# Kernel tuning notes

Measured on AMD Instinct MI355X. Metric: run time of the kernel, lower is better.

Reference implementation:

```python
import jax, jax.numpy as jnp
import numpy as np

B, C, S, H, W = 1, 256, 64, 32, 128
BLOCKS, HEADS, DH = 2, 8, 32
SCALE = DH ** (-0.5)


def layer_norm(x, w, b, eps=1e-5):
    mu = jnp.mean(x, axis=-1, keepdims=True)
    var = jnp.var(x, axis=-1, keepdims=True)
    return (x - mu) * jax.lax.rsqrt(var + eps) * w + b


def generate_y_for_attn(y, u):
    # y: (B,C,H,W), u: (B,S,S) float -> (B, S^2, 2H, C)
    Bv, Cv, Hv, Wv = y.shape
    Sv = u.shape[1]
    uf = jnp.floor(u).reshape(Bv, Sv * Sv)
    u_left = jnp.clip(uf, 0, Wv - 1).astype(jnp.int32)
    u_right = jnp.clip(uf + 1, 0, Wv - 1).astype(jnp.int32)
    yf = y.reshape(Bv, Cv * Hv, Wv)

    def gather_w(idx):
        idxb = jnp.broadcast_to(idx[:, None, :], (Bv, Cv * Hv, Sv * Sv))
        return jnp.take_along_axis(yf, idxb, axis=2).reshape(Bv, Cv, Hv, Sv * Sv)

    ys = jnp.concatenate([gather_w(u_left), gather_w(u_right)], axis=2)  # (B,C,2H,S2)
    return ys.transpose(0, 3, 2, 1)  # (B, S2, 2H, C)


def cross_attention(x, y, p, i):
    # x: (B,M,C), y: (B,M,N,C)
    q = layer_norm(x, p['ln_q_w'][i], p['ln_q_b'][i]) @ p['Wq'][i]        # (B,M,HD)
    k = layer_norm(y, p['ln_k_w'][i], p['ln_k_b'][i]) @ p['Wk'][i]        # (B,M,N,HD)
    v = layer_norm(y, p['ln_v_w'][i], p['ln_v_b'][i]) @ p['Wv'][i]        # (B,M,N,HD)
    Bv, M, _ = q.shape
    N = k.shape[2]
    q = q.reshape(Bv, M, HEADS, DH)
    k = k.reshape(Bv, M, N, HEADS, DH)
    v = v.reshape(Bv, M, N, HEADS, DH)
    dot = SCALE * jnp.einsum('bmhd,bmnhd->bhmn', q, k)                    # (B,H,M,N)
    attn = jax.nn.softmax(dot, axis=-1)
    a = jnp.einsum('bhmn,bmnhd->bmhd', attn, v).reshape(Bv, M, HEADS * DH)
    z = a @ p['Wproj'][i] + p['bproj'][i]
    z = layer_norm(z, p['ln_pre_w'][i], p['ln_pre_b'][i])
    h = jax.nn.gelu(z @ p['Wm1'][i] + p['bm1'][i], approximate=False)
    z = z + (h @ p['Wm2'][i] + p['bm2'][i])
    return layer_norm(z, p['ln_post_w'][i], p['ln_post_b'][i])


def setup_inputs() -> dict:
    key = jax.random.key(0)
    ks = jax.random.split(key, 16)
    std = 0.02
    inp = {
        'grd2sat': jax.random.normal(ks[0], (B, C, S, S), jnp.float32),
        'grd_x': jax.random.normal(ks[1], (B, C, H, W), jnp.float32),
        'u': jax.random.uniform(ks[2], (B, S, S), jnp.float32) * (W - 1),
        'ln_q_w': jnp.ones((BLOCKS, C)), 'ln_q_b': jnp.zeros((BLOCKS, C)),
        'ln_k_w': jnp.ones((BLOCKS, C)), 'ln_k_b': jnp.zeros((BLOCKS, C)),
        'ln_v_w': jnp.ones((BLOCKS, C)), 'ln_v_b': jnp.zeros((BLOCKS, C)),
        'Wq': std * jax.random.normal(ks[3], (BLOCKS, C, HEADS * DH)),
        'Wk': std * jax.random.normal(ks[4], (BLOCKS, C, HEADS * DH)),
        'Wv': std * jax.random.normal(ks[5], (BLOCKS, C, HEADS * DH)),
        'Wproj': std * jax.random.normal(ks[6], (BLOCKS, HEADS * DH, C)),
        'bproj': jnp.zeros((BLOCKS, C)),
        'ln_pre_w': jnp.ones((BLOCKS, C)), 'ln_pre_b': jnp.zeros((BLOCKS, C)),
        'Wm1': std * jax.random.normal(ks[7], (BLOCKS, C, 2 * C)),
        'bm1': jnp.zeros((BLOCKS, 2 * C)),
        'Wm2': std * jax.random.normal(ks[8], (BLOCKS, 2 * C, C)),
        'bm2': jnp.zeros((BLOCKS, C)),
        'ln_post_w': jnp.ones((BLOCKS, C)), 'ln_post_b': jnp.zeros((BLOCKS, C)),
    }
    return inp


def reference(grd2sat, grd_x, u, ln_q_w, ln_q_b, ln_k_w, ln_k_b, ln_v_w, ln_v_b,
              Wq, Wk, Wv, Wproj, bproj, ln_pre_w, ln_pre_b, Wm1, bm1, Wm2, bm2,
              ln_post_w, ln_post_b):
    p = dict(ln_q_w=ln_q_w, ln_q_b=ln_q_b, ln_k_w=ln_k_w, ln_k_b=ln_k_b,
             ln_v_w=ln_v_w, ln_v_b=ln_v_b, Wq=Wq, Wk=Wk, Wv=Wv, Wproj=Wproj,
             bproj=bproj, ln_pre_w=ln_pre_w, ln_pre_b=ln_pre_b, Wm1=Wm1, bm1=bm1,
             Wm2=Wm2, bm2=bm2, ln_post_w=ln_post_w, ln_post_b=ln_post_b)
    y_attn = generate_y_for_attn(grd_x, u)               # (B, S^2, 2H, C)
    x = grd2sat.reshape(B, C, S * S).transpose(0, 2, 1)  # (B, M, C)
    for i in range(BLOCKS):
        # (Swin self-attention layer omitted; cross-attention stack only.)
        x = cross_attention(x, y_attn, p, i)
    out = x.transpose(0, 2, 1).reshape(B, C, S, S)
    # L2 normalize over channel dim
    norm = jnp.sqrt(jnp.sum(out * out, axis=1, keepdims=True))
    return out / jnp.maximum(norm, 1e-12)
```

## Files before the change

kernel.cpp:

```cpp
#include <hip/hip_runtime.h>
#include <math.h>


#define C_DIM 256
#define M_DIM 4096
#define W_DIM 128
#define H_DIM 32
#define ATT_SCALE 0.17677669529663687f

typedef __attribute__((ext_vector_type(8))) short short8;
typedef __attribute__((ext_vector_type(4))) short short4v;
typedef __attribute__((ext_vector_type(4))) float floatx4;

__device__ __forceinline__ unsigned short f2bf(float f) {
    unsigned u = __float_as_uint(f);
    unsigned r = (u + 0x7fffu + ((u >> 16) & 1u)) >> 16;
    return (unsigned short)r;
}
__device__ __forceinline__ float gelu_exact(float x) {
    return 0.5f * x * (1.0f + erff(x * 0.70710678118654752f));
}

struct PrepArgs {
    const float* grd2sat; float* xcur;
    const float* grd_x;   float* yhat;
    const float* u; int* perm; int4* chunks; int* nchunks;
    const float* win[12]; unsigned short* wout[12]; const float* wlnw[12];
    int wR[12], wC[12], wbase[13];
    const float* fW[10]; const float* flnb[10]; const float* fbase[10];
    float* fout[10];
    int fN[10], fwcol[10], focol[10];
};

__global__ __launch_bounds__(256) void prep_kernel(PrepArgs a) {
    __shared__ float smemf[9024];
    int b = blockIdx.x, t = threadIdx.x;
    if (b < 256) {
        float (*tile)[65] = (float(*)[65])smemf;
        int m0 = (b & 63) << 6, c0 = (b >> 6) << 6;
        for (int it = 0; it < 16; ++it) {
            int idx = it * 256 + t;
            int co = idx >> 6, mo = idx & 63;
            tile[co][mo] = a.grd2sat[(size_t)(c0 + co) * M_DIM + m0 + mo];
        }
        __syncthreads();
        for (int it = 0; it < 16; ++it) {
            int idx = it * 256 + t;
            int mo = idx >> 6, co = idx & 63;
            a.xcur[(size_t)(m0 + mo) * C_DIM + c0 + co] = tile[co][mo];
        }
    } else if (b < 384) {
        int idx = b - 256;
        int h = idx & 31, w0 = (idx >> 5) << 5;
        float (*tile)[33] = (float(*)[33])smemf;
        float (*ps)[32] = (float(*)[32])(smemf + 8448);
        float (*pss)[32] = (float(*)[32])(smemf + 8704);
        float* mu_s = smemf + 8960;
        float* rs_s = smemf + 8992;
        int wo = t & 31, cb = t >> 5;
        for (int it = 0; it < 32; ++it) {
            int c = it * 8 + cb;
            tile[c][wo] = a.grd_x[(size_t)c * (H_DIM * W_DIM) + h * W_DIM + w0 + wo];
        }
        __syncthreads();
        {
            int w = t & 31, part = t >> 5;
            float s = 0.f, ss = 0.f;
            for (int c = part * 32; c < part * 32 + 32; ++c) {
                float x = tile[c][w];
                s += x; ss += x * x;
            }
            ps[part][w] = s; pss[part][w] = ss;
        }
        __syncthreads();
        if (t < 32) {
            float s = 0.f, ss = 0.f;
            for (int p = 0; p < 8; ++p) { s += ps[p][t]; ss += pss[p][t]; }
            float mu = s * (1.f / 256.f);
            float var = ss * (1.f / 256.f) - mu * mu;
            mu_s[t] = mu;
            rs_s[t] = rsqrtf(var + 1e-5f);
        }
        __syncthreads();
        for (int jj = 0; jj < 32; ++jj) {
            float mu = mu_s[jj], rs = rs_s[jj];
            a.yhat[((size_t)(w0 + jj) * H_DIM + h) * C_DIM + t] =
                (tile[t][jj] - mu) * rs;
        }
    } else if (b < 1408) {
        int wI = b - 384;
        int e = 0;
        while (wI >= a.wbase[e + 1]) ++e;
        int tl = wI - a.wbase[e];
        int tilesC = a.wC[e] >> 5;
        int tr = tl / tilesC, tc = tl - tr * tilesC;
        int r0 = tr << 5, c0 = tc << 5;
        const float* in = a.win[e];
        unsigned short* out = a.wout[e];
        const float* lnw = a.wlnw[e];
        int R = a.wR[e], Cc = a.wC[e];
        float (*tile)[33] = (float(*)[33])smemf;
        int rl = t >> 3, cq = (t & 7) << 2;
        float4 v = *(const float4*)&in[(size_t)(r0 + rl) * Cc + c0 + cq];
        if (lnw) {
            float s = lnw[r0 + rl];
            v.x *= s; v.y *= s; v.z *= s; v.w *= s;
        }
        tile[rl][cq + 0] = v.x;
        tile[rl][cq + 1] = v.y;
        tile[rl][cq + 2] = v.z;
        tile[rl][cq + 3] = v.w;
        __syncthreads();
        int cl = t >> 3, rq = (t & 7) << 2;
        ushort4 o;
        o.x = f2bf(tile[rq + 0][cl]);
        o.y = f2bf(tile[rq + 1][cl]);
        o.z = f2bf(tile[rq + 2][cl]);
        o.w = f2bf(tile[rq + 3][cl]);
        *(ushort4*)&out[(size_t)(c0 + cl) * R + r0 + rq] = o;
    } else if (b < 1418) {
        int jj = b - 1408;
        int N = a.fN[jj];
        int wcol = a.fwcol[jj] + t;
        const float* W = a.fW[jj];
        const float* lb = a.flnb[jj];
        float s = a.fbase[jj] ? a.fbase[jj][wcol] : 0.f;
        for (int k = 0; k < 256; ++k) s += lb[k] * W[(size_t)k * N + wcol];
        a.fout[jj][a.focol[jj] + t] = s;
    } else {
        int* hist = (int*)smemf;
        int* cur = (int*)smemf + 128;
        unsigned short* wlb = (unsigned short*)((int*)smemf + 256);
        if (t < 128) hist[t] = 0;
        __syncthreads();
        for (int it = 0; it < 16; ++it) {
            int m = it * 256 + t;
            int wl = (int)floorf(a.u[m]);
            wl = max(0, min(wl, 126));
            wlb[m] = (unsigned short)wl;
            atomicAdd(&hist[wl], 1);
        }
        __syncthreads();
        if (t == 0) {
            int run = 0, nc = 0;
            for (int bkt = 0; bkt < 127; ++bkt) {
                int c = hist[bkt];
                cur[bkt] = run;
                int q0 = run;
                while (c > 0) {
                    int take = min(c, 32);
                    a.chunks[nc] = make_int4(bkt, q0, take, 0);
                    ++nc; q0 += take; c -= take;
                }
                run += hist[bkt];
            }
            *a.nchunks = nc;
        }
        __syncthreads();
        for (int it = 0; it < 16; ++it) {
            int m = it * 256 + t;
            int wl = wlb[m];
            int pos = atomicAdd(&cur[wl], 1);
            a.perm[pos] = m;
        }
    }
}

struct GJ {
    const void* A; const unsigned short* Bt;
    const float* bias; const float* aw; const float* ab;
    const float* rw; const float* rb; const float* res;
    float* wrz; void* out; unsigned short* out2;
    int K, N;
};

template <int LN, int EPI, int OUTM, bool WRZ, bool ABF16>
__device__ __forceinline__ void gemm_core(const GJ& j, short (*As)[264],
                                          short (*Bs)[264], int bm, int by) {
    int t = threadIdx.x;
    int bn = by << 6;
    int wv = t >> 6, lane = t & 63;
    int mt = wv & 1, nt0 = (wv >> 1) << 1;
    int quad = lane >> 4, l16 = lane & 15;
    floatx4 acc0 = {0.f, 0.f, 0.f, 0.f};
    floatx4 acc1 = {0.f, 0.f, 0.f, 0.f};
    const int K = j.K;
    for (int kc = 0; kc < K; kc += 256) {
        if (kc) __syncthreads();
        if (ABF16) {
            int ar = t >> 3, cq = (t & 7) << 5;
            const unsigned short* ap =
                (const unsigned short*)j.A + (size_t)(bm + ar) * K + kc + cq;
#pragma unroll
            for (int c = 0; c < 4; ++c)
                *(uint4*)&As[ar][cq + (c << 3)] = *(const uint4*)(ap + (c << 3));
        } else {
            int ar = t >> 3, cq = (t & 7) << 2;
            const float* ap = (const float*)j.A + (size_t)(bm + ar) * K + kc + cq;
            float4 v[8];
#pragma unroll
            for (int g = 0; g < 8; ++g) v[g] = *(const float4*)(ap + g * 32);
            if (LN >= 1) {
                float s = 0.f, ss = 0.f;
#pragma unroll
                for (int g = 0; g < 8; ++g) {
                    s += v[g].x + v[g].y + v[g].z + v[g].w;
                    ss += v[g].x * v[g].x + v[g].y * v[g].y + v[g].z * v[g].z +
                          v[g].w * v[g].w;
                }
#pragma unroll
                for (int o = 1; o < 8; o <<= 1) {
                    s += __shfl_xor(s, o, 64);
                    ss += __shfl_xor(ss, o, 64);
                }
                float mu = s * (1.f / 256.f);
                float rs = rsqrtf(ss * (1.f / 256.f) - mu * mu + 1e-5f);
#pragma unroll
                for (int g = 0; g < 8; ++g) {
                    v[g].x = (v[g].x - mu) * rs;
                    v[g].y = (v[g].y - mu) * rs;
                    v[g].z = (v[g].z - mu) * rs;
                    v[g].w = (v[g].w - mu) * rs;
                }
                if (LN == 2) {
                    float s2 = 0.f, ss2 = 0.f;
#pragma unroll
                    for (int g = 0; g < 8; ++g) {
                        float4 w4 = *(const float4*)(j.aw + cq + g * 32);
                        float4 b4 = *(const float4*)(j.ab + cq + g * 32);
                        v[g].x = v[g].x * w4.x + b4.x;
                        v[g].y = v[g].y * w4.y + b4.y;
                        v[g].z = v[g].z * w4.z + b4.z;
                        v[g].w = v[g].w * w4.w + b4.w;
                        s2 += v[g].x + v[g].y + v[g].z + v[g].w;
                        ss2 += v[g].x * v[g].x + v[g].y * v[g].y +
                               v[g].z * v[g].z + v[g].w * v[g].w;
                    }
#pragma unroll
                    for (int o = 1; o < 8; o <<= 1) {
                        s2 += __shfl_xor(s2, o, 64);
                        ss2 += __shfl_xor(ss2, o, 64);
                    }
                    float mu2 = s2 * (1.f / 256.f);
                    float rs2 = rsqrtf(ss2 * (1.f / 256.f) - mu2 * mu2 + 1e-5f);
#pragma unroll
                    for (int g = 0; g < 8; ++g) {
                        v[g].x = (v[g].x - mu2) * rs2;
                        v[g].y = (v[g].y - mu2) * rs2;
                        v[g].z = (v[g].z - mu2) * rs2;
                        v[g].w = (v[g].w - mu2) * rs2;
                    }
                }
            }
            if (WRZ) {
                if (by == 0) {
#pragma unroll
                    for (int g = 0; g < 8; ++g)
                        *(float4*)&j.wrz[(size_t)(bm + ar) * 256 + cq + g * 32] =
                            v[g];
                }
            }
#pragma unroll
            for (int g = 0; g < 8; ++g) {
                short4v o;
                o[0] = (short)f2bf(v[g].x);
                o[1] = (short)f2bf(v[g].y);
                o[2] = (short)f2bf(v[g].z);
                o[3] = (short)f2bf(v[g].w);
                *(short4v*)&As[ar][cq + g * 32] = o;
            }
        }
        {
            int br = t >> 2, cq2 = (t & 3) << 3;
            const unsigned short* bp = j.Bt + (size_t)(bn + br) * K + kc + cq2;
#pragma unroll
            for (int g = 0; g < 8; ++g)
                *(short8*)&Bs[br][cq2 + g * 32] = *(const short8*)(bp + g * 32);
        }
        __syncthreads();
#pragma unroll
        for (int k0 = 0; k0 < 8; ++k0) {
            short8 aa = *(const short8*)&As[(mt << 4) + l16][(k0 << 5) + (quad << 3)];
            short8 b0 = *(const short8*)&Bs[(nt0 << 4) + l16][(k0 << 5) + (quad << 3)];
            short8 b1 =
                *(const short8*)&Bs[((nt0 + 1) << 4) + l16][(k0 << 5) + (quad << 3)];
            acc0 = __builtin_amdgcn_mfma_f32_16x16x32_bf16(aa, b0, acc0, 0, 0, 0);
            acc1 = __builtin_amdgcn_mfma_f32_16x16x32_bf16(aa, b1, acc1, 0, 0, 0);
        }
    }
#pragma unroll
    for (int jj = 0; jj < 2; ++jj) {
        const floatx4 accv = jj ? acc1 : acc0;
        int col = bn + ((nt0 + jj) << 4) + l16;
        float bv = j.bias ? j.bias[col] : 0.f;
#pragma unroll
        for (int r = 0; r < 4; ++r) {
            int row = bm + (mt << 4) + (quad << 2) + r;
            float v = accv[r] + bv;
            if (EPI == 1) v = gelu_exact(v);
            if (EPI == 2)
                v += j.res[(size_t)row * 256 + col] * j.rw[col] + j.rb[col];
            if (OUTM == 0) {
                ((float*)j.out)[(size_t)row * j.N + col] = v;
            } else if (OUTM == 1) {
                ((unsigned short*)j.out)[(size_t)row * j.N + col] = f2bf(v);
            } else {
                if (col < 256)
                    ((unsigned short*)j.out)[(size_t)row * 256 + col] = f2bf(v);
                else
                    j.out2[(size_t)(col - 256) * M_DIM + row] = f2bf(v);
            }
        }
    }
}

template <int MODE>
__global__ __launch_bounds__(256) void gemm_mode(GJ j0, GJ j1, GJ j2) {
    __shared__ short As[32][264];
    __shared__ short Bs[64][264];
    int bm = blockIdx.x << 5;
    if (MODE == 0) {
        if ((int)blockIdx.y < 4)
            gemm_core<1, 0, 1, false, false>(j0, As, Bs, bm, blockIdx.y);
        else if ((int)blockIdx.y < 12)
            gemm_core<0, 0, 2, false, false>(j1, As, Bs, bm, blockIdx.y - 4);
        else
            gemm_core<0, 0, 2, false, false>(j2, As, Bs, bm, blockIdx.y - 12);
    } else if (MODE == 1) {
        gemm_core<2, 0, 1, false, false>(j0, As, Bs, bm, blockIdx.y);
    } else if (MODE == 2) {
        gemm_core<0, 0, 0, false, true>(j0, As, Bs, bm, blockIdx.y);
    } else if (MODE == 3) {
        gemm_core<1, 1, 1, true, false>(j0, As, Bs, bm, blockIdx.y);
    } else {
        gemm_core<0, 2, 0, false, true>(j0, As, Bs, bm, blockIdx.y);
    }
}

__global__ __launch_bounds__(256) void attn_kernel(
    const unsigned short* __restrict__ Qb, const unsigned short* __restrict__ Kt,
    const unsigned short* __restrict__ Vt, const int* __restrict__ perm,
    const int4* __restrict__ chunks, const int* __restrict__ nchunks,
    unsigned short* __restrict__ Ao) {
    __shared__ float S[32][69];
    __shared__ short Pb[32][72];
    __shared__ int gperm[32];
    if ((int)blockIdx.x >= *nchunks) return;
    int4 cd = chunks[blockIdx.x];
    int wl = cd.x, qstart = cd.y, qcnt = cd.z;
    int t = threadIdx.x;
    if (t < 32) gperm[t] = (t < qcnt) ? perm[qstart + t] : perm[qstart];
    __syncthreads();
    int wv = t >> 6, lane = t & 63, quad = lane >> 4, l16 = lane & 15;
    int mt = wv & 1, nt0 = (wv >> 1) << 1;
    int ntP = wv >> 1;
    const unsigned short* qp = Qb + (size_t)gperm[(mt << 4) + l16] * 256;
    const unsigned short* kp0 =
        Kt + ((size_t)((wl << 5) + (nt0 << 4) + l16)) * 256;
    const unsigned short* kp1 = kp0 + (16 * 256);
    int sq = t >> 3, sg = t & 7;
    int hb = (int)blockIdx.y << 2;
#pragma unroll 1
    for (int h = hb; h < hb + 4; ++h) {
        {
            short8 aa = *(const short8*)(qp + (h << 5) + (quad << 3));
            short8 b0 = *(const short8*)(kp0 + (h << 5) + (quad << 3));
            short8 b1 = *(const short8*)(kp1 + (h << 5) + (quad << 3));
            floatx4 z = {0.f, 0.f, 0.f, 0.f};
            floatx4 c0 = __builtin_amdgcn_mfma_f32_16x16x32_bf16(aa, b0, z, 0, 0, 0);
            floatx4 c1 = __builtin_amdgcn_mfma_f32_16x16x32_bf16(aa, b1, z, 0, 0, 0);
#pragma unroll
            for (int r = 0; r < 4; ++r) {
                int row = (mt << 4) + (quad << 2) + r;
                S[row][(nt0 << 4) + l16] = c0[r];
                S[row][((nt0 + 1) << 4) + l16] = c1[r];
            }
        }
        __syncthreads();
        {
            float e[8];
            float s = 0.f;
#pragma unroll
            for (int c = 0; c < 8; ++c) {
                e[c] = __expf(S[sq][(sg << 3) + c] * ATT_SCALE);
                s += e[c];
            }
            s += __shfl_xor(s, 1, 64);
            s += __shfl_xor(s, 2, 64);
            s += __shfl_xor(s, 4, 64);
            float ri = 1.f / s;
#pragma unroll
            for (int c = 0; c < 8; ++c)
                Pb[sq][(sg << 3) + c] = (short)f2bf(e[c] * ri);
        }
        __syncthreads();
        {
            const unsigned short* vp =
                Vt + ((size_t)((h << 5) + (ntP << 4) + l16)) * M_DIM + (wl << 5);
            floatx4 acc = {0.f, 0.f, 0.f, 0.f};
#pragma unroll
            for (int ks = 0; ks < 2; ++ks) {
                short8 pa =
                    *(const short8*)&Pb[(mt << 4) + l16][(ks << 5) + (quad << 3)];
                short8 vb = *(const short8*)(vp + (ks << 5) + (quad << 3));
                acc = __builtin_amdgcn_mfma_f32_16x16x32_bf16(pa, vb, acc, 0, 0, 0);
            }
#pragma unroll
            for (int r = 0; r < 4; ++r) {
                int q = (mt << 4) + (quad << 2) + r;
                if (q < qcnt)
                    Ao[(size_t)gperm[q] * 256 + (h << 5) + (ntP << 4) + l16] =
                        f2bf(acc[r]);
            }
        }
    }
}

__global__ __launch_bounds__(256) void out_kernel(const float* __restrict__ X,
                                                  const float* __restrict__ w,
                                                  const float* __restrict__ b,
                                                  float* __restrict__ out) {
    __shared__ float tile[64][65];
    int t = threadIdx.x;
    int mo = t >> 2, q = t & 3;
    int m0 = blockIdx.x << 6;
    const float* p = X + (size_t)(m0 + mo) * C_DIM + (q << 6);
    float4 v[16];
    float s = 0.f, ss = 0.f;
#pragma unroll
    for (int c = 0; c < 16; ++c) {
        v[c] = *(const float4*)(p + c * 4);
        s += v[c].x + v[c].y + v[c].z + v[c].w;
        ss += v[c].x * v[c].x + v[c].y * v[c].y + v[c].z * v[c].z + v[c].w * v[c].w;
    }
    s += __shfl_xor(s, 1, 64); s += __shfl_xor(s, 2, 64);
    ss += __shfl_xor(ss, 1, 64); ss += __shfl_xor(ss, 2, 64);
    float mu = s * (1.f / 256.f);
    float rs = rsqrtf(ss * (1.f / 256.f) - mu * mu + 1e-5f);
    float ss2 = 0.f;
#pragma unroll
    for (int c = 0; c < 16; ++c) {
        float4 w4 = *(const float4*)&w[(q << 6) + c * 4];
        float4 b4 = *(const float4*)&b[(q << 6) + c * 4];
        v[c].x = (v[c].x - mu) * rs * w4.x + b4.x;
        v[c].y = (v[c].y - mu) * rs * w4.y + b4.y;
        v[c].z = (v[c].z - mu) * rs * w4.z + b4.z;
        v[c].w = (v[c].w - mu) * rs * w4.w + b4.w;
        ss2 += v[c].x * v[c].x + v[c].y * v[c].y + v[c].z * v[c].z + v[c].w * v[c].w;
    }
    ss2 += __shfl_xor(ss2, 1, 64); ss2 += __shfl_xor(ss2, 2, 64);
    float sc = 1.f / fmaxf(sqrtf(ss2), 1e-12f);
    for (int cc = 0; cc < 4; ++cc) {
        if (q == cc) {
#pragma unroll
            for (int c = 0; c < 16; ++c) {
                tile[mo][c * 4 + 0] = v[c].x * sc;
                tile[mo][c * 4 + 1] = v[c].y * sc;
                tile[mo][c * 4 + 2] = v[c].z * sc;
                tile[mo][c * 4 + 3] = v[c].w * sc;
            }
        }
        __syncthreads();
        for (int it = 0; it < 16; ++it) {
            int idx = it * 256 + t;
            int co = idx >> 6, mr = idx & 63;
            out[(size_t)((cc << 6) + co) * M_DIM + m0 + mr] = tile[mr][co];
        }
        __syncthreads();
    }
}

extern "C" void kernel_launch(void* const* d_in, const int* in_sizes, int n_in,
                              void* d_out, int out_size, void* d_ws, size_t ws_size,
                              hipStream_t stream) {
    const float* grd2sat = (const float*)d_in[0];
    const float* grd_x   = (const float*)d_in[1];
    const float* u       = (const float*)d_in[2];
    const float* ln_q_w  = (const float*)d_in[3];
    const float* ln_q_b  = (const float*)d_in[4];
    const float* ln_k_w  = (const float*)d_in[5];
    const float* ln_k_b  = (const float*)d_in[6];
    const float* ln_v_w  = (const float*)d_in[7];
    const float* ln_v_b  = (const float*)d_in[8];
    const float* Wq      = (const float*)d_in[9];
    const float* Wk      = (const float*)d_in[10];
    const float* Wv      = (const float*)d_in[11];
    const float* Wproj   = (const float*)d_in[12];
    const float* bproj   = (const float*)d_in[13];
    const float* ln_pre_w = (const float*)d_in[14];
    const float* ln_pre_b = (const float*)d_in[15];
    const float* Wm1     = (const float*)d_in[16];
    const float* bm1     = (const float*)d_in[17];
    const float* Wm2     = (const float*)d_in[18];
    const float* bm2     = (const float*)d_in[19];
    const float* ln_post_w = (const float*)d_in[20];
    const float* ln_post_b = (const float*)d_in[21];

    float* ws   = (float*)d_ws;
    float* yhat = ws;
    float* xcur = ws + 1048576;
    float* zq   = ws + 2097152;
    float* zbuf = ws + 3145728;
    unsigned short* hbuf = (unsigned short*)(ws + 4194304);
    unsigned short* Qb   = (unsigned short*)(ws + 5242880);
    unsigned short* abuf = (unsigned short*)(ws + 5767168);
    unsigned short* Ktab0 = (unsigned short*)(ws + 6291456);
    unsigned short* Vt0   = (unsigned short*)(ws + 6815744);
    unsigned short* Ktab1 = (unsigned short*)(ws + 7340032);
    unsigned short* Vt1   = (unsigned short*)(ws + 7864320);
    unsigned short* Bt    = (unsigned short*)(ws + 8388608);
    float* biasbuf = ws + 8912896;
    int*  perm    = (int*)(ws + 8915456);
    int4* chunks  = (int4*)(ws + 8919552);
    int*  nchunks = (int*)(ws + 8921600);
    const size_t BS = 524288;
    const size_t OQ = 0, OKV = 65536, OP = 196608, OM1 = 262144, OM2 = 393216;

    dim3 b256(256);

    PrepArgs pa;
    pa.grd2sat = grd2sat; pa.xcur = xcur;
    pa.grd_x = grd_x;     pa.yhat = yhat;
    pa.u = u; pa.perm = perm; pa.chunks = chunks; pa.nchunks = nchunks;
    {
        int base = 0;
        for (int i = 0; i < 2; ++i) {
            int e = 6 * i;
            unsigned short* bt = Bt + i * BS;
            pa.win[e+0] = Wq + i * 65536;    pa.wout[e+0] = bt + OQ;
            pa.wlnw[e+0] = ln_q_w + i * 256; pa.wR[e+0] = 256; pa.wC[e+0] = 256;
            pa.win[e+1] = Wk + i * 65536;    pa.wout[e+1] = bt + OKV;
            pa.wlnw[e+1] = ln_k_w + i * 256; pa.wR[e+1] = 256; pa.wC[e+1] = 256;
            pa.win[e+2] = Wv + i * 65536;    pa.wout[e+2] = bt + OKV + 65536;
            pa.wlnw[e+2] = ln_v_w + i * 256; pa.wR[e+2] = 256; pa.wC[e+2] = 256;
            pa.win[e+3] = Wproj + i * 65536; pa.wout[e+3] = bt + OP;
            pa.wlnw[e+3] = nullptr;          pa.wR[e+3] = 256; pa.wC[e+3] = 256;
            pa.win[e+4] = Wm1 + i * 131072;  pa.wout[e+4] = bt + OM1;
            pa.wlnw[e+4] = ln_pre_w + i * 256; pa.wR[e+4] = 256; pa.wC[e+4] = 512;
            pa.win[e+5] = Wm2 + i * 131072;  pa.wout[e+5] = bt + OM2;
            pa.wlnw[e+5] = nullptr;          pa.wR[e+5] = 512; pa.wC[e+5] = 256;
        }
        for (int e = 0; e < 12; ++e) {
            pa.wbase[e] = base;
            base += (pa.wR[e] >> 5) * (pa.wC[e] >> 5);
        }
        pa.wbase[12] = base;
        for (int i = 0; i < 2; ++i) {
            int jb = 5 * i;
            float* bb = biasbuf + i * 1280;
            pa.fW[jb+0] = Wq + i * 65536; pa.flnb[jb+0] = ln_q_b + i * 256;
            pa.fbase[jb+0] = nullptr; pa.fout[jb+0] = bb;
            pa.fN[jb+0] = 256; pa.fwcol[jb+0] = 0; pa.focol[jb+0] = 0;
            pa.fW[jb+1] = Wk + i * 65536; pa.flnb[jb+1] = ln_k_b + i * 256;
            pa.fbase[jb+1] = nullptr; pa.fout[jb+1] = bb + 256;
            pa.fN[jb+1] = 256; pa.fwcol[jb+1] = 0; pa.focol[jb+1] = 0;
            pa.fW[jb+2] = Wv + i * 65536; pa.flnb[jb+2] = ln_v_b + i * 256;
            pa.fbase[jb+2] = nullptr; pa.fout[jb+2] = bb + 256;
            pa.fN[jb+2] = 256; pa.fwcol[jb+2] = 0; pa.focol[jb+2] = 256;
            pa.fW[jb+3] = Wm1 + i * 131072; pa.flnb[jb+3] = ln_pre_b + i * 256;
            pa.fbase[jb+3] = bm1 + i * 512; pa.fout[jb+3] = bb + 768;
            pa.fN[jb+3] = 512; pa.fwcol[jb+3] = 0; pa.focol[jb+3] = 0;
            pa.fW[jb+4] = Wm1 + i * 131072; pa.flnb[jb+4] = ln_pre_b + i * 256;
            pa.fbase[jb+4] = bm1 + i * 512; pa.fout[jb+4] = bb + 768;
            pa.fN[jb+4] = 512; pa.fwcol[jb+4] = 256; pa.focol[jb+4] = 256;
        }
    }
    prep_kernel<<<1419, b256, 0, stream>>>(pa);

    GJ jz = {};
    for (int i = 0; i < 2; ++i) {
        const unsigned short* bt = Bt + i * BS;
        float* bb = biasbuf + i * 1280;
        unsigned short* Kt = i ? Ktab1 : Ktab0;
        unsigned short* Vt = i ? Vt1 : Vt0;

        GJ jq = {};
        jq.A = xcur; jq.Bt = bt + OQ; jq.bias = bb;
        if (i == 1) { jq.aw = ln_post_w; jq.ab = ln_post_b; }
        jq.out = Qb; jq.K = 256; jq.N = 256;
        if (i == 0) {
            GJ jkv0 = {};
            jkv0.A = yhat; jkv0.Bt = Bt + OKV; jkv0.bias = biasbuf + 256;
            jkv0.out = Ktab0; jkv0.out2 = Vt0; jkv0.K = 256; jkv0.N = 512;
            GJ jkv1 = {};
            jkv1.A = yhat; jkv1.Bt = Bt + BS + OKV; jkv1.bias = biasbuf + 1280 + 256;
            jkv1.out = Ktab1; jkv1.out2 = Vt1; jkv1.K = 256; jkv1.N = 512;
            gemm_mode<0><<<dim3(128, 20), b256, 0, stream>>>(jq, jkv0, jkv1);
        } else {
            gemm_mode<1><<<dim3(128, 4), b256, 0, stream>>>(jq, jz, jz);
        }

        attn_kernel<<<dim3(384, 2), b256, 0, stream>>>(Qb, Kt, Vt, perm, chunks,
                                                       nchunks, abuf);

        GJ jp = {};
        jp.A = abuf; jp.Bt = bt + OP; jp.bias = bproj + i * 256;
        jp.out = zq; jp.K = 256; jp.N = 256;
        gemm_mode<2><<<dim3(128, 4), b256, 0, stream>>>(jp, jz, jz);

        GJ jm1 = {};
        jm1.A = zq; jm1.Bt = bt + OM1; jm1.bias = bb + 768;
        jm1.out = hbuf; jm1.wrz = zbuf; jm1.K = 256; jm1.N = 512;
        gemm_mode<3><<<dim3(128, 8), b256, 0, stream>>>(jm1, jz, jz);

        GJ jm2 = {};
        jm2.A = hbuf; jm2.Bt = bt + OM2; jm2.bias = bm2 + i * 256;
        jm2.res = zbuf; jm2.rw = ln_pre_w + i * 256; jm2.rb = ln_pre_b + i * 256;
        jm2.out = xcur; jm2.K = 512; jm2.N = 256;
        gemm_mode<4><<<dim3(128, 4), b256, 0, stream>>>(jm2, jz, jz);
    }
    out_kernel<<<64, b256, 0, stream>>>(xcur, ln_post_w + 256, ln_post_b + 256,
                                        (float*)d_out);
}
```

Before: 215.7 us.

## Fuse Q-proj, attention, out-proj and MLP for both blocks into one megakernel

Replaces the per-block chain of Q GEMM, attention, projection GEMM, MLP1 and MLP2 launches with a single kernel. Each workgroup owns a chunk of up to 32 query rows that share a window and keeps all intermediates in LDS across both blocks. K/V projections for both blocks are computed up front in a separate kernel. This removes many launches and the global round trips for Q, attention output, z and h. In exchange it uses about 147KB of LDS per workgroup, so occupancy is one workgroup per CU, and only 288 workgroups run, each reloading the full weight matrices.

Result: slower. 238.4 us (+10.5%).

```diff
diff --git a/kernel.cpp b/kernel.cpp
--- a/kernel.cpp
+++ b/kernel.cpp
@@ -222,43 +222,6 @@
                     v[g].z = (v[g].z - mu) * rs;
                     v[g].w = (v[g].w - mu) * rs;
                 }
-                if (LN == 2) {
-                    float s2 = 0.f, ss2 = 0.f;
-#pragma unroll
-                    for (int g = 0; g < 8; ++g) {
-                        float4 w4 = *(const float4*)(j.aw + cq + g * 32);
-                        float4 b4 = *(const float4*)(j.ab + cq + g * 32);
-                        v[g].x = v[g].x * w4.x + b4.x;
-                        v[g].y = v[g].y * w4.y + b4.y;
-                        v[g].z = v[g].z * w4.z + b4.z;
-                        v[g].w = v[g].w * w4.w + b4.w;
-                        s2 += v[g].x + v[g].y + v[g].z + v[g].w;
-                        ss2 += v[g].x * v[g].x + v[g].y * v[g].y +
-                               v[g].z * v[g].z + v[g].w * v[g].w;
-                    }
-#pragma unroll
-                    for (int o = 1; o < 8; o <<= 1) {
-                        s2 += __shfl_xor(s2, o, 64);
-                        ss2 += __shfl_xor(ss2, o, 64);
-                    }
-                    float mu2 = s2 * (1.f / 256.f);
-                    float rs2 = rsqrtf(ss2 * (1.f / 256.f) - mu2 * mu2 + 1e-5f);
-#pragma unroll
-                    for (int g = 0; g < 8; ++g) {
-                        v[g].x = (v[g].x - mu2) * rs2;
-                        v[g].y = (v[g].y - mu2) * rs2;
-                        v[g].z = (v[g].z - mu2) * rs2;
-                        v[g].w = (v[g].w - mu2) * rs2;
-                    }
-                }
-            }
-            if (WRZ) {
-                if (by == 0) {
-#pragma unroll
-                    for (int g = 0; g < 8; ++g)
-                        *(float4*)&j.wrz[(size_t)(bm + ar) * 256 + cq + g * 32] =
-                            v[g];
-                }
             }
 #pragma unroll
             for (int g = 0; g < 8; ++g) {
@@ -297,9 +260,6 @@
         for (int r = 0; r < 4; ++r) {
             int row = bm + (mt << 4) + (quad << 2) + r;
             float v = accv[r] + bv;
-            if (EPI == 1) v = gelu_exact(v);
-            if (EPI == 2)
-                v += j.res[(size_t)row * 256 + col] * j.rw[col] + j.rb[col];
             if (OUTM == 0) {
                 ((float*)j.out)[(size_t)row * j.N + col] = v;
             } else if (OUTM == 1) {
@@ -314,105 +274,368 @@
     }
 }
 
-template <int MODE>
-__global__ __launch_bounds__(256) void gemm_mode(GJ j0, GJ j1, GJ j2) {
+__global__ __launch_bounds__(256) void kv_kernel(GJ j0, GJ j1) {
     __shared__ short As[32][264];
     __shared__ short Bs[64][264];
     int bm = blockIdx.x << 5;
-    if (MODE == 0) {
-        if ((int)blockIdx.y < 4)
-            gemm_core<1, 0, 1, false, false>(j0, As, Bs, bm, blockIdx.y);
-        else if ((int)blockIdx.y < 12)
-            gemm_core<0, 0, 2, false, false>(j1, As, Bs, bm, blockIdx.y - 4);
-        else
-            gemm_core<0, 0, 2, false, false>(j2, As, Bs, bm, blockIdx.y - 12);
-    } else if (MODE == 1) {
-        gemm_core<2, 0, 1, false, false>(j0, As, Bs, bm, blockIdx.y);
-    } else if (MODE == 2) {
-        gemm_core<0, 0, 0, false, true>(j0, As, Bs, bm, blockIdx.y);
-    } else if (MODE == 3) {
-        gemm_core<1, 1, 1, true, false>(j0, As, Bs, bm, blockIdx.y);
-    } else {
-        gemm_core<0, 2, 0, false, true>(j0, As, Bs, bm, blockIdx.y);
-    }
+    if ((int)blockIdx.y < 8)
+        gemm_core<0, 0, 2, false, false>(j0, As, Bs, bm, blockIdx.y);
+    else
+        gemm_core<0, 0, 2, false, false>(j1, As, Bs, bm, blockIdx.y - 8);
 }
 
-__global__ __launch_bounds__(256) void attn_kernel(
-    const unsigned short* __restrict__ Qb, const unsigned short* __restrict__ Kt,
-    const unsigned short* __restrict__ Vt, const int* __restrict__ perm,
-    const int4* __restrict__ chunks, const int* __restrict__ nchunks,
-    unsigned short* __restrict__ Ao) {
-    __shared__ float S[32][69];
-    __shared__ short Pb[32][72];
-    __shared__ int gperm[32];
-    if ((int)blockIdx.x >= *nchunks) return;
-    int4 cd = chunks[blockIdx.x];
+struct MegaArgs {
+    const float* xcur;
+    const int* perm; const int4* chunks; const int* nchunks;
+    float* xfinal;
+    const unsigned short* Wq[2]; const unsigned short* Wp[2];
+    const unsigned short* Wm1[2]; const unsigned short* Wm2[2];
+    const unsigned short* Ktb[2]; const unsigned short* Vtb[2];
+    const float* qb[2]; const float* m1b[2];
+    const float* bpj[2]; const float* bm2v[2];
+    const float* pw[2]; const float* pb[2];
+    const float* aw; const float* ab;
+};
+
+__device__ __forceinline__ void cg_pass(const short* As, int lda,
+                                        const unsigned short* Bt, int K, int bn,
+                                        short (*Bst)[264], floatx4& acc0,
+                                        floatx4& acc1) {
+    int t = threadIdx.x;
+    int wv = t >> 6, lane = t & 63, quad = lane >> 4, l16 = lane & 15;
+    int mt = wv & 1, nt0 = (wv >> 1) << 1;
+    int br = t >> 2, cq2 = (t & 3) << 3;
+#pragma unroll 1
+    for (int kc = 0; kc < K; kc += 256) {
+        const unsigned short* bp = Bt + (size_t)(bn + br) * K + kc + cq2;
+#pragma unroll
+        for (int g = 0; g < 8; ++g)
+            *(short8*)&Bst[br][cq2 + (g << 5)] = *(const short8*)(bp + (g << 5));
+        __syncthreads();
+        const short* ap = As + (size_t)((mt << 4) + l16) * lda + kc + (quad << 3);
+#pragma unroll
+        for (int k0 = 0; k0 < 8; ++k0) {
+            short8 aa = *(const short8*)(ap + (k0 << 5));
+            short8 b0 =
+                *(const short8*)&Bst[(nt0 << 4) + l16][(k0 << 5) + (quad << 3)];
+            short8 b1 =
+                *(const short8*)&Bst[((nt0 + 1) << 4) + l16][(k0 << 5) + (quad << 3)];
+            acc0 = __builtin_amdgcn_mfma_f32_16x16x32_bf16(aa, b0, acc0, 0, 0, 0);
+            acc1 = __builtin_amdgcn_mfma_f32_16x16x32_bf16(aa, b1, acc1, 0, 0, 0);
+        }
+        __syncthreads();
+    }
+}
+
+__global__ __launch_bounds__(256) void mega_kernel(MegaArgs a) {
+    __shared__ __align__(16) char smem[150656];
+    short (*XH)[264] = (short(*)[264])(smem);
+    short (*HH)[520] = (short(*)[520])(smem);
+    short (*QR)[264] = (short(*)[264])(smem + 33280);
+    float (*Zf)[260] = (float(*)[260])(smem + 33280);
+    short (*ZH)[264] = (short(*)[264])(smem + 66560);
+    short (*AR)[264] = (short(*)[264])(smem + 83456);
+    float (*XO)[260] = (float(*)[260])(smem + 83456);
+    short (*Bst)[264] = (short(*)[264])(smem + 116736);
+    float (*SS)[69] = (float(*)[69])(smem + 116736);
+    short (*PB)[72] = (short(*)[72])(smem + 116736 + 8832);
+    int* gp = (int*)(smem + 150528);
+
+    if ((int)blockIdx.x >= *a.nchunks) return;
+    int4 cd = a.chunks[blockIdx.x];
     int wl = cd.x, qstart = cd.y, qcnt = cd.z;
     int t = threadIdx.x;
-    if (t < 32) gperm[t] = (t < qcnt) ? perm[qstart + t] : perm[qstart];
+    if (t < 32) gp[t] = (t < qcnt) ? a.perm[qstart + t] : a.perm[qstart];
     __syncthreads();
+
     int wv = t >> 6, lane = t & 63, quad = lane >> 4, l16 = lane & 15;
-    int mt = wv & 1, nt0 = (wv >> 1) << 1;
-    int ntP = wv >> 1;
-    const unsigned short* qp = Qb + (size_t)gperm[(mt << 4) + l16] * 256;
-    const unsigned short* kp0 =
-        Kt + ((size_t)((wl << 5) + (nt0 << 4) + l16)) * 256;
-    const unsigned short* kp1 = kp0 + (16 * 256);
-    int sq = t >> 3, sg = t & 7;
-    int hb = (int)blockIdx.y << 2;
+    int mt = wv & 1, nt0 = (wv >> 1) << 1, ntP = wv >> 1;
+    int r8 = t >> 3, cq = (t & 7) << 5;
+    int sg = t & 7;
+
 #pragma unroll 1
-    for (int h = hb; h < hb + 4; ++h) {
+    for (int l = 0; l < 2; ++l) {
         {
-            short8 aa = *(const short8*)(qp + (h << 5) + (quad << 3));
-            short8 b0 = *(const short8*)(kp0 + (h << 5) + (quad << 3));
-            short8 b1 = *(const short8*)(kp1 + (h << 5) + (quad << 3));
-            floatx4 z = {0.f, 0.f, 0.f, 0.f};
-            floatx4 c0 = __builtin_amdgcn_mfma_f32_16x16x32_bf16(aa, b0, z, 0, 0, 0);
-            floatx4 c1 = __builtin_amdgcn_mfma_f32_16x16x32_bf16(aa, b1, z, 0, 0, 0);
-#pragma unroll
-            for (int r = 0; r < 4; ++r) {
-                int row = (mt << 4) + (quad << 2) + r;
-                S[row][(nt0 << 4) + l16] = c0[r];
-                S[row][((nt0 + 1) << 4) + l16] = c1[r];
-            }
-        }
-        __syncthreads();
+            float4 v[8];
+            if (l == 0) {
+                const float* xp = a.xcur + (size_t)gp[r8] * 256 + cq;
+#pragma unroll
+                for (int g = 0; g < 8; ++g) v[g] = *(const float4*)(xp + (g << 2));
+            } else {
+#pragma unroll
+                for (int g = 0; g < 8; ++g)
+                    v[g] = *(const float4*)&XO[r8][cq + (g << 2)];
+            }
+            float s = 0.f, ss = 0.f;
+#pragma unroll
+            for (int g = 0; g < 8; ++g) {
+                s += v[g].x + v[g].y + v[g].z + v[g].w;
+                ss += v[g].x * v[g].x + v[g].y * v[g].y + v[g].z * v[g].z +
+                      v[g].w * v[g].w;
+            }
+#pragma unroll
+            for (int o = 1; o < 8; o <<= 1) {
+                s += __shfl_xor(s, o, 64);
+                ss += __shfl_xor(ss, o, 64);
+            }
+            float mu = s * (1.f / 256.f);
+            float rs = rsqrtf(ss * (1.f / 256.f) - mu * mu + 1e-5f);
+#pragma unroll
+            for (int g = 0; g < 8; ++g) {
+                v[g].x = (v[g].x - mu) * rs;
+                v[g].y = (v[g].y - mu) * rs;
+                v[g].z = (v[g].z - mu) * rs;
+                v[g].w = (v[g].w - mu) * rs;
+            }
+            if (l == 1) {
+                float s2 = 0.f, ss2 = 0.f;
+#pragma unroll
+                for (int g = 0; g < 8; ++g) {
+                    float4 w4 = *(const float4*)&a.aw[cq + (g << 2)];
+                    float4 b4 = *(const float4*)&a.ab[cq + (g << 2)];
+                    v[g].x = v[g].x * w4.x + b4.x;
+                    v[g].y = v[g].y * w4.y + b4.y;
+                    v[g].z = v[g].z * w4.z + b4.z;
+                    v[g].w = v[g].w * w4.w + b4.w;
+                    s2 += v[g].x + v[g].y + v[g].z + v[g].w;
+                    ss2 += v[g].x * v[g].x + v[g].y * v[g].y + v[g].z * v[g].z +
+                           v[g].w * v[g].w;
+                }
+#pragma unroll
+                for (int o = 1; o < 8; o <<= 1) {
+                    s2 += __shfl_xor(s2, o, 64);
+                    ss2 += __shfl_xor(ss2, o, 64);
+                }
+                float mu2 = s2 * (1.f / 256.f);
+                float rs2 = rsqrtf(ss2 * (1.f / 256.f) - mu2 * mu2 + 1e-5f);
+#pragma unroll
+                for (int g = 0; g < 8; ++g) {
+                    v[g].x = (v[g].x - mu2) * rs2;
+                    v[g].y = (v[g].y - mu2) * rs2;
+                    v[g].z = (v[g].z - mu2) * rs2;
+                    v[g].w = (v[g].w - mu2) * rs2;
+                }
+            }
+#pragma unroll
+            for (int g = 0; g < 8; ++g) {
+                short4v o;
+                o[0] = (short)f2bf(v[g].x);
+                o[1] = (short)f2bf(v[g].y);
+                o[2] = (short)f2bf(v[g].z);
+                o[3] = (short)f2bf(v[g].w);
+                *(short4v*)&XH[r8][cq + (g << 2)] = o;
+            }
+        }
+        __syncthreads();
+
         {
-            float e[8];
-            float s = 0.f;
-#pragma unroll
-            for (int c = 0; c < 8; ++c) {
-                e[c] = __expf(S[sq][(sg << 3) + c] * ATT_SCALE);
-                s += e[c];
-            }
-            s += __shfl_xor(s, 1, 64);
-            s += __shfl_xor(s, 2, 64);
-            s += __shfl_xor(s, 4, 64);
-            float ri = 1.f / s;
-#pragma unroll
-            for (int c = 0; c < 8; ++c)
-                Pb[sq][(sg << 3) + c] = (short)f2bf(e[c] * ri);
-        }
-        __syncthreads();
+            const float* qb = a.qb[l];
+#pragma unroll 1
+            for (int bn = 0; bn < 256; bn += 64) {
+                floatx4 a0 = {0.f, 0.f, 0.f, 0.f};
+                floatx4 a1 = {0.f, 0.f, 0.f, 0.f};
+                cg_pass((const short*)XH, 264, a.Wq[l], 256, bn, Bst, a0, a1);
+#pragma unroll
+                for (int jj = 0; jj < 2; ++jj) {
+                    const floatx4 av = jj ? a1 : a0;
+                    int col = bn + ((nt0 + jj) << 4) + l16;
+                    float bv = qb[col];
+#pragma unroll
+                    for (int r = 0; r < 4; ++r)
+                        QR[(mt << 4) + (quad << 2) + r][col] =
+                            (short)f2bf(av[r] + bv);
+                }
+            }
+        }
+        __syncthreads();
+
         {
-            const unsigned short* vp =
-                Vt + ((size_t)((h << 5) + (ntP << 4) + l16)) * M_DIM + (wl << 5);
-            floatx4 acc = {0.f, 0.f, 0.f, 0.f};
-#pragma unroll
-            for (int ks = 0; ks < 2; ++ks) {
-                short8 pa =
-                    *(const short8*)&Pb[(mt << 4) + l16][(ks << 5) + (quad << 3)];
-                short8 vb = *(const short8*)(vp + (ks << 5) + (quad << 3));
-                acc = __builtin_amdgcn_mfma_f32_16x16x32_bf16(pa, vb, acc, 0, 0, 0);
-            }
-#pragma unroll
-            for (int r = 0; r < 4; ++r) {
-                int q = (mt << 4) + (quad << 2) + r;
-                if (q < qcnt)
-                    Ao[(size_t)gperm[q] * 256 + (h << 5) + (ntP << 4) + l16] =
-                        f2bf(acc[r]);
-            }
-        }
+            const unsigned short* kp0 =
+                a.Ktb[l] + ((size_t)((wl << 5) + (nt0 << 4) + l16)) * 256;
+            const unsigned short* kp1 = kp0 + (16 * 256);
+            const unsigned short* vpb =
+                a.Vtb[l] + (size_t)((ntP << 4) + l16) * M_DIM + (wl << 5);
+            short8 qa = *(const short8*)&QR[(mt << 4) + l16][(quad << 3)];
+            short8 kb0 = *(const short8*)(kp0 + (quad << 3));
+            short8 kb1 = *(const short8*)(kp1 + (quad << 3));
+            short8 va0 = *(const short8*)(vpb + (quad << 3));
+            short8 va1 = *(const short8*)(vpb + 32 + (quad << 3));
+#pragma unroll 1
+            for (int h = 0; h < 8; ++h) {
+                {
+                    floatx4 zz = {0.f, 0.f, 0.f, 0.f};
+                    floatx4 c0 =
+                        __builtin_amdgcn_mfma_f32_16x16x32_bf16(qa, kb0, zz, 0, 0, 0);
+                    floatx4 c1 =
+                        __builtin_amdgcn_mfma_f32_16x16x32_bf16(qa, kb1, zz, 0, 0, 0);
+#pragma unroll
+                    for (int r = 0; r < 4; ++r) {
+                        int row = (mt << 4) + (quad << 2) + r;
+                        SS[row][(nt0 << 4) + l16] = c0[r];
+                        SS[row][((nt0 + 1) << 4) + l16] = c1[r];
+                    }
+                }
+                short8 nva0 = va0, nva1 = va1;
+                if (h < 7) {
+                    int hn = h + 1;
+                    qa = *(const short8*)&QR[(mt << 4) + l16][(hn << 5) + (quad << 3)];
+                    kb0 = *(const short8*)(kp0 + (hn << 5) + (quad << 3));
+                    kb1 = *(const short8*)(kp1 + (hn << 5) + (quad << 3));
+                    const unsigned short* vpn = vpb + (size_t)(hn << 5) * M_DIM;
+                    nva0 = *(const short8*)(vpn + (quad << 3));
+                    nva1 = *(const short8*)(vpn + 32 + (quad << 3));
+                }
+                __syncthreads();
+                {
+                    float e[8];
+                    float s = 0.f;
+#pragma unroll
+                    for (int c = 0; c < 8; ++c) {
+                        e[c] = __expf(SS[r8][(sg << 3) + c] * ATT_SCALE);
+                        s += e[c];
+                    }
+                    s += __shfl_xor(s, 1, 64);
+                    s += __shfl_xor(s, 2, 64);
+                    s += __shfl_xor(s, 4, 64);
+                    float ri = 1.f / s;
+#pragma unroll
+                    for (int c = 0; c < 8; ++c)
+                        PB[r8][(sg << 3) + c] = (short)f2bf(e[c] * ri);
+                }
+                __syncthreads();
+                {
+                    floatx4 acc = {0.f, 0.f, 0.f, 0.f};
+#pragma unroll
+                    for (int ks = 0; ks < 2; ++ks) {
+                        short8 pa = *(const short8*)&PB[(mt << 4) + l16]
+                                                      [(ks << 5) + (quad << 3)];
+                        short8 vb = ks ? va1 : va0;
+                        acc = __builtin_amdgcn_mfma_f32_16x16x32_bf16(pa, vb, acc,
+                                                                      0, 0, 0);
+                    }
+#pragma unroll
+                    for (int r = 0; r < 4; ++r)
+                        AR[(mt << 4) + (quad << 2) + r]
+                          [(h << 5) + (ntP << 4) + l16] = (short)f2bf(acc[r]);
+                }
+                va0 = nva0;
+                va1 = nva1;
+            }
+        }
+        __syncthreads();
+
+        {
+            const float* bpj = a.bpj[l];
+#pragma unroll 1
+            for (int bn = 0; bn < 256; bn += 64) {
+                floatx4 a0 = {0.f, 0.f, 0.f, 0.f};
+                floatx4 a1 = {0.f, 0.f, 0.f, 0.f};
+                cg_pass((const short*)AR, 264, a.Wp[l], 256, bn, Bst, a0, a1);
+#pragma unroll
+                for (int jj = 0; jj < 2; ++jj) {
+                    const floatx4 av = jj ? a1 : a0;
+                    int col = bn + ((nt0 + jj) << 4) + l16;
+                    float bv = bpj[col];
+#pragma unroll
+                    for (int r = 0; r < 4; ++r)
+                        Zf[(mt << 4) + (quad << 2) + r][col] = av[r] + bv;
+                }
+            }
+        }
+        __syncthreads();
+
+        {
+            const float* pw = a.pw[l];
+            const float* pb = a.pb[l];
+            float4 v[8];
+#pragma unroll
+            for (int g = 0; g < 8; ++g) v[g] = *(const float4*)&Zf[r8][cq + (g << 2)];
+            float s = 0.f, ss = 0.f;
+#pragma unroll
+            for (int g = 0; g < 8; ++g) {
+                s += v[g].x + v[g].y + v[g].z + v[g].w;
+                ss += v[g].x * v[g].x + v[g].y * v[g].y + v[g].z * v[g].z +
+                      v[g].w * v[g].w;
+            }
+#pragma unroll
+            for (int o = 1; o < 8; o <<= 1) {
+                s += __shfl_xor(s, o, 64);
+                ss += __shfl_xor(ss, o, 64);
+            }
+            float mu = s * (1.f / 256.f);
+            float rs = rsqrtf(ss * (1.f / 256.f) - mu * mu + 1e-5f);
+#pragma unroll
+            for (int g = 0; g < 8; ++g) {
+                float4 z;
+                z.x = (v[g].x - mu) * rs;
+                z.y = (v[g].y - mu) * rs;
+                z.z = (v[g].z - mu) * rs;
+                z.w = (v[g].w - mu) * rs;
+                short4v o;
+                o[0] = (short)f2bf(z.x);
+                o[1] = (short)f2bf(z.y);
+                o[2] = (short)f2bf(z.z);
+                o[3] = (short)f2bf(z.w);
+                *(short4v*)&ZH[r8][cq + (g << 2)] = o;
+                float4 w4 = *(const float4*)&pw[cq + (g << 2)];
+                float4 b4 = *(const float4*)&pb[cq + (g << 2)];
+                float4 za;
+                za.x = z.x * w4.x + b4.x;
+                za.y = z.y * w4.y + b4.y;
+                za.z = z.z * w4.z + b4.z;
+                za.w = z.w * w4.w + b4.w;
+                *(float4*)&Zf[r8][cq + (g << 2)] = za;
+            }
+        }
+        __syncthreads();
+
+        {
+            const float* m1b = a.m1b[l];
+#pragma unroll 1
+            for (int bn = 0; bn < 512; bn += 64) {
+                floatx4 a0 = {0.f, 0.f, 0.f, 0.f};
+                floatx4 a1 = {0.f, 0.f, 0.f, 0.f};
+                cg_pass((const short*)ZH, 264, a.Wm1[l], 256, bn, Bst, a0, a1);
+#pragma unroll
+                for (int jj = 0; jj < 2; ++jj) {
+                    const floatx4 av = jj ? a1 : a0;
+                    int col = bn + ((nt0 + jj) << 4) + l16;
+                    float bv = m1b[col];
+#pragma unroll
+                    for (int r = 0; r < 4; ++r)
+                        HH[(mt << 4) + (quad << 2) + r][col] =
+                            (short)f2bf(gelu_exact(av[r] + bv));
+                }
+            }
+        }
+        __syncthreads();
+
+        {
+            const float* b2 = a.bm2v[l];
+#pragma unroll 1
+            for (int bn = 0; bn < 256; bn += 64) {
+                floatx4 a0 = {0.f, 0.f, 0.f, 0.f};
+                floatx4 a1 = {0.f, 0.f, 0.f, 0.f};
+                cg_pass((const short*)HH, 520, a.Wm2[l], 512, bn, Bst, a0, a1);
+#pragma unroll
+                for (int jj = 0; jj < 2; ++jj) {
+                    const floatx4 av = jj ? a1 : a0;
+                    int col = bn + ((nt0 + jj) << 4) + l16;
+                    float bv = b2[col];
+#pragma unroll
+                    for (int r = 0; r < 4; ++r) {
+                        int row = (mt << 4) + (quad << 2) + r;
+                        float v = av[r] + bv + Zf[row][col];
+                        if (l == 0) {
+                            XO[row][col] = v;
+                        } else if (row < qcnt) {
+                            a.xfinal[(size_t)gp[row] * 256 + col] = v;
+                        }
+                    }
+                }
+            }
+        }
+        __syncthreads();
     }
 }
 
@@ -500,10 +723,6 @@
     float* yhat = ws;
     float* xcur = ws + 1048576;
     float* zq   = ws + 2097152;
-    float* zbuf = ws + 3145728;
-    unsigned short* hbuf = (unsigned short*)(ws + 4194304);
-    unsigned short* Qb   = (unsigned short*)(ws + 5242880);
-    unsigned short* abuf = (unsigned short*)(ws + 5767168);
     unsigned short* Ktab0 = (unsigned short*)(ws + 6291456);
     unsigned short* Vt0   = (unsigned short*)(ws + 6815744);
     unsigned short* Ktab1 = (unsigned short*)(ws + 7340032);
@@ -567,48 +786,32 @@
     }
     prep_kernel<<<1419, b256, 0, stream>>>(pa);
 
-    GJ jz = {};
+    GJ jkv0 = {};
+    jkv0.A = yhat; jkv0.Bt = Bt + OKV; jkv0.bias = biasbuf + 256;
+    jkv0.out = Ktab0; jkv0.out2 = Vt0; jkv0.K = 256; jkv0.N = 512;
+    GJ jkv1 = {};
+    jkv1.A = yhat; jkv1.Bt = Bt + BS + OKV; jkv1.bias = biasbuf + 1280 + 256;
+    jkv1.out = Ktab1; jkv1.out2 = Vt1; jkv1.K = 256; jkv1.N = 512;
+    kv_kernel<<<dim3(128, 16), b256, 0, stream>>>(jkv0, jkv1);
+
+    MegaArgs ma;
+    ma.xcur = xcur; ma.perm = perm; ma.chunks = chunks; ma.nchunks = nchunks;
+    ma.xfinal = zq;
     for (int i = 0; i < 2; ++i) {
         const unsigned short* bt = Bt + i * BS;
-        float* bb = biasbuf + i * 1280;
-        unsigned short* Kt = i ? Ktab1 : Ktab0;
-        unsigned short* Vt = i ? Vt1 : Vt0;
-
-        GJ jq = {};
-        jq.A = xcur; jq.Bt = bt + OQ; jq.bias = bb;
-        if (i == 1) { jq.aw = ln_post_w; jq.ab = ln_post_b; }
-        jq.out = Qb; jq.K = 256; jq.N = 256;
-        if (i == 0) {
-            GJ jkv0 = {};
-            jkv0.A = yhat; jkv0.Bt = Bt + OKV; jkv0.bias = biasbuf + 256;
-            jkv0.out = Ktab0; jkv0.out2 = Vt0; jkv0.K = 256; jkv0.N = 512;
-            GJ jkv1 = {};
-            jkv1.A = yhat; jkv1.Bt = Bt + BS + OKV; jkv1.bias = biasbuf + 1280 + 256;
-            jkv1.out = Ktab1; jkv1.out2 = Vt1; jkv1.K = 256; jkv1.N = 512;
-            gemm_mode<0><<<dim3(128, 20), b256, 0, stream>>>(jq, jkv0, jkv1);
-        } else {
-            gemm_mode<1><<<dim3(128, 4), b256, 0, stream>>>(jq, jz, jz);
-        }
-
-        attn_kernel<<<dim3(384, 2), b256, 0, stream>>>(Qb, Kt, Vt, perm, chunks,
-                                                       nchunks, abuf);
-
-        GJ jp = {};
-        jp.A = abuf; jp.Bt = bt + OP; jp.bias = bproj + i * 256;
-        jp.out = zq; jp.K = 256; jp.N = 256;
-        gemm_mode<2><<<dim3(128, 4), b256, 0, stream>>>(jp, jz, jz);
-
-        GJ jm1 = {};
-        jm1.A = zq; jm1.Bt = bt + OM1; jm1.bias = bb + 768;
-        jm1.out = hbuf; jm1.wrz = zbuf; jm1.K = 256; jm1.N = 512;
-        gemm_mode<3><<<dim3(128, 8), b256, 0, stream>>>(jm1, jz, jz);
-
-        GJ jm2 = {};
-        jm2.A = hbuf; jm2.Bt = bt + OM2; jm2.bias = bm2 + i * 256;
-        jm2.res = zbuf; jm2.rw = ln_pre_w + i * 256; jm2.rb = ln_pre_b + i * 256;
-        jm2.out = xcur; jm2.K = 512; jm2.N = 256;
-        gemm_mode<4><<<dim3(128, 4), b256, 0, stream>>>(jm2, jz, jz);
-    }
-    out_kernel<<<64, b256, 0, stream>>>(xcur, ln_post_w + 256, ln_post_b + 256,
+        ma.Wq[i] = bt + OQ; ma.Wp[i] = bt + OP;
+        ma.Wm1[i] = bt + OM1; ma.Wm2[i] = bt + OM2;
+        ma.Ktb[i] = i ? Ktab1 : Ktab0; ma.Vtb[i] = i ? Vt1 : Vt0;
+        ma.qb[i] = biasbuf + i * 1280;
+        ma.m1b[i] = biasbuf + i * 1280 + 768;
+        ma.bpj[i] = bproj + i * 256;
+        ma.bm2v[i] = bm2 + i * 256;
+        ma.pw[i] = ln_pre_w + i * 256;
+        ma.pb[i] = ln_pre_b + i * 256;
+    }
+    ma.aw = ln_post_w; ma.ab = ln_post_b;
+    mega_kernel<<<288, b256, 0, stream>>>(ma);
+
+    out_kernel<<<64, b256, 0, stream>>>(zq, ln_post_w + 256, ln_post_b + 256,
                                         (float*)d_out);
 }
```
